# Performance work log

Measured on AMD Instinct MI355X. Metric: run time of the kernel, lower is better.

Reference implementation:

```python
import jax, jax.numpy as jnp
import numpy as np

H = 1024

def setup_inputs() -> dict:
    key = jax.random.key(0)
    ks = jax.random.split(key, 9)
    s = 1.0 / np.sqrt(H)
    x = jax.random.normal(ks[0], (4, 2048, H), dtype=jnp.float32)
    Wq = jax.random.uniform(ks[1], (H, H), jnp.float32, -s, s)
    bq = jax.random.uniform(ks[2], (H,), jnp.float32, -s, s)
    Wk = jax.random.uniform(ks[3], (H, H), jnp.float32, -s, s)
    bk = jax.random.uniform(ks[4], (H,), jnp.float32, -s, s)
    Wv = jax.random.uniform(ks[5], (H, H), jnp.float32, -s, s)
    bv = jax.random.uniform(ks[6], (H,), jnp.float32, -s, s)
    Wo = jax.random.uniform(ks[7], (H, H), jnp.float32, -s, s)
    bo = jax.random.uniform(ks[8], (H,), jnp.float32, -s, s)
    return {"x": x, "Wq": Wq, "bq": bq, "Wk": Wk, "bk": bk,
            "Wv": Wv, "bv": bv, "Wo": Wo, "bo": bo}

def reference(x, Wq, bq, Wk, bk, Wv, bv, Wo, bo):
    # Linear uses y = x @ W.T + b (torch convention: W is [out, in])
    q = jnp.einsum('bsd,ed->bse', x, Wq) + bq
    k = jnp.einsum('bsd,ed->bse', x, Wk) + bk
    v = jnp.einsum('bsd,ed->bse', x, Wv) + bv
    scale = q.shape[-1] ** 0.5
    attn = jnp.einsum('bqe,bke->bqk', q, k) / scale  # [B,S,S]
    attn = jax.nn.softmax(attn, axis=-1)
    out = jnp.einsum('bqk,bke->bqe', attn, v)
    return jnp.einsum('bse,oe->bso', out, Wo) + bo
```

## Files before the change

kernel.cpp:

```cpp
#include <hip/hip_runtime.h>

typedef short  short4v __attribute__((ext_vector_type(4)));
typedef short  short8v __attribute__((ext_vector_type(8)));
typedef __bf16 bf16x8  __attribute__((ext_vector_type(8)));
typedef float  f32x4   __attribute__((ext_vector_type(4)));
typedef float  float4v __attribute__((ext_vector_type(4)));

__device__ __forceinline__ short f2bf(float f) {
  unsigned u = __builtin_bit_cast(unsigned, f);
  u += 0x7fffu + ((u >> 16) & 1u);
  return (short)(u >> 16);
}
__device__ __forceinline__ float bf2f(short h) {
  unsigned u = ((unsigned)(unsigned short)h) << 16;
  return __builtin_bit_cast(float, u);
}
__device__ __forceinline__ bf16x8 ld8(const short* p) {
  return __builtin_bit_cast(bf16x8, *reinterpret_cast<const short8v*>(p));
}

__constant__ const float kExpScale = 0.04508422f;

__global__ __launch_bounds__(256) void k_cvt(const float* __restrict__ in,
                                             short* __restrict__ out) {
  const int i = blockIdx.x * 256 + threadIdx.x;
#pragma unroll
  for (int j = 0; j < 4; ++j) {
    const long g = (long)i + (long)j * 524288;
    float4v v = *reinterpret_cast<const float4v*>(in + g * 4);
    short4v o;
    o[0] = f2bf(v[0]); o[1] = f2bf(v[1]); o[2] = f2bf(v[2]); o[3] = f2bf(v[3]);
    *reinterpret_cast<short4v*>(out + g * 4) = o;
  }
}

__global__ __launch_bounds__(256) void k_wprep(const float* __restrict__ i0,
    const float* __restrict__ i1, const float* __restrict__ i2,
    const float* __restrict__ i3, short* __restrict__ o0, short* __restrict__ o1,
    short* __restrict__ o2, short* __restrict__ o3) {
  const int z = blockIdx.z;
  const float* in = z == 0 ? i0 : z == 1 ? i1 : z == 2 ? i2 : i3;
  short* out = z == 0 ? o0 : z == 1 ? o1 : z == 2 ? o2 : o3;
  const float sc = (z == 1) ? kExpScale : 1.0f;
  const int tid = threadIdx.x;
  const int c0 = blockIdx.x << 6;
  const int r0 = blockIdx.y << 7;
  if (z == 3) {
#pragma unroll
    for (int j = 0; j < 8; ++j) {
      int idx = j * 256 + tid;
      int r = idx >> 4, c4 = (idx & 15) << 2;
      float4v v = *reinterpret_cast<const float4v*>(in + (long)(r0 + r) * 1024 + c0 + c4);
      short4v o;
      o[0] = f2bf(v[0]); o[1] = f2bf(v[1]); o[2] = f2bf(v[2]); o[3] = f2bf(v[3]);
      *reinterpret_cast<short4v*>(out + (long)(r0 + r) * 1024 + c0 + c4) = o;
    }
    return;
  }
  __shared__ float tile[128][65];
#pragma unroll
  for (int j = 0; j < 8; ++j) {
    int idx = j * 256 + tid;
    int r = idx >> 4, c4 = (idx & 15) << 2;
    float4v v = *reinterpret_cast<const float4v*>(in + (long)(r0 + r) * 1024 + c0 + c4);
    tile[r][c4 + 0] = v[0] * sc; tile[r][c4 + 1] = v[1] * sc;
    tile[r][c4 + 2] = v[2] * sc; tile[r][c4 + 3] = v[3] * sc;
  }
  __syncthreads();
#pragma unroll
  for (int j = 0; j < 8; ++j) {
    int idx = j * 256 + tid;
    int rO = idx >> 5, g4 = (idx & 31) << 2;
    short4v o;
    o[0] = f2bf(tile[g4 + 0][rO]); o[1] = f2bf(tile[g4 + 1][rO]);
    o[2] = f2bf(tile[g4 + 2][rO]); o[3] = f2bf(tile[g4 + 3][rO]);
    *reinterpret_cast<short4v*>(out + (long)(c0 + rO) * 1024 + r0 + g4) = o;
  }
}

__device__ __forceinline__ void gemm_loop(const short* __restrict__ Ab,
    const short* __restrict__ Bb, int K, int lda, int ldb, int bm, int bn,
    f32x4 (&acc)[4][4]) {
  __shared__ __align__(16) short lsA[128 * 64];
  __shared__ __align__(16) short lsB[128 * 64];
  const int tid = threadIdx.x;
  const int lane = tid & 63, wid = tid >> 6;
  const int wr = wid >> 1, wc = wid & 1;
  const int fr = lane & 15, fq = lane >> 4;
  for (int kt = 0; kt < K; kt += 64) {
    __syncthreads();
#pragma unroll
    for (int c = 0; c < 4; ++c) {
      const int idx = c * 256 + tid;
      const int row = idx >> 3, colh = (idx & 7) << 3;
      const short* ga = Ab + (long)(bm + row) * lda + kt + colh;
      const short* gb = Bb + (long)(bn + row) * ldb + kt + colh;
      __builtin_amdgcn_global_load_lds(
          (const __attribute__((address_space(1))) void*)ga,
          (__attribute__((address_space(3))) void*)&lsA[idx * 8], 16, 0, 0);
      __builtin_amdgcn_global_load_lds(
          (const __attribute__((address_space(1))) void*)gb,
          (__attribute__((address_space(3))) void*)&lsB[idx * 8], 16, 0, 0);
    }
    __syncthreads();
#pragma unroll
    for (int ks = 0; ks < 64; ks += 32) {
      bf16x8 a[4], b[4];
#pragma unroll
      for (int m = 0; m < 4; ++m)
        a[m] = ld8(&lsA[(wr * 64 + m * 16 + fr) * 64 + ks + fq * 8]);
#pragma unroll
      for (int n = 0; n < 4; ++n)
        b[n] = ld8(&lsB[(wc * 64 + n * 16 + fr) * 64 + ks + fq * 8]);
#pragma unroll
      for (int m = 0; m < 4; ++m)
#pragma unroll
        for (int n = 0; n < 4; ++n)
          acc[m][n] = __builtin_amdgcn_mfma_f32_16x16x32_bf16(a[m], b[n], acc[m][n], 0, 0, 0);
    }
  }
}

__device__ __forceinline__ void gemm_loop_w(const short* __restrict__ Ab,
    const short* __restrict__ Bb, int K, int lda, int ldb, int bm, int bn,
    f32x4 (&acc)[4][4]) {
  __shared__ __align__(16) short lsA[128 * 64];
  __shared__ __align__(16) short lsB[256 * 64];
  const int tid = threadIdx.x;
  const int lane = tid & 63, wid = tid >> 6;
  const int wr = wid >> 2, wc = wid & 3;
  const int fr = lane & 15, fq = lane >> 4;
  for (int kt = 0; kt < K; kt += 64) {
    __syncthreads();
#pragma unroll
    for (int c = 0; c < 2; ++c) {
      const int idx = c * 512 + tid;
      const int row = idx >> 3, colh = (idx & 7) << 3;
      __builtin_amdgcn_global_load_lds(
          (const __attribute__((address_space(1))) void*)
              (Ab + (long)(bm + row) * lda + kt + colh),
          (__attribute__((address_space(3))) void*)&lsA[idx * 8], 16, 0, 0);
    }
#pragma unroll
    for (int c = 0; c < 4; ++c) {
      const int idx = c * 512 + tid;
      const int row = idx >> 3, colh = (idx & 7) << 3;
      __builtin_amdgcn_global_load_lds(
          (const __attribute__((address_space(1))) void*)
              (Bb + (long)(bn + row) * ldb + kt + colh),
          (__attribute__((address_space(3))) void*)&lsB[idx * 8], 16, 0, 0);
    }
    __syncthreads();
#pragma unroll
    for (int ks = 0; ks < 64; ks += 32) {
      bf16x8 a[4], b[4];
#pragma unroll
      for (int m = 0; m < 4; ++m)
        a[m] = ld8(&lsA[(wr * 64 + m * 16 + fr) * 64 + ks + fq * 8]);
#pragma unroll
      for (int n = 0; n < 4; ++n)
        b[n] = ld8(&lsB[(wc * 64 + n * 16 + fr) * 64 + ks + fq * 8]);
#pragma unroll
      for (int m = 0; m < 4; ++m)
#pragma unroll
        for (int n = 0; n < 4; ++n)
          acc[m][n] = __builtin_amdgcn_mfma_f32_16x16x32_bf16(a[m], b[n], acc[m][n], 0, 0, 0);
    }
  }
}

__global__ __launch_bounds__(256, 3) void k_prep2(
    const short* __restrict__ wkT, const short* __restrict__ wqT,
    const short* __restrict__ wob, const short* __restrict__ wvT,
    const float* __restrict__ bq, const float* __restrict__ Wo,
    const float* __restrict__ bv,
    short* __restrict__ mt, short* __restrict__ wv2,
    float* __restrict__ bvec, float* __restrict__ bvp) {
  const int tid = threadIdx.x;
  const int lane = tid & 63, wid = tid >> 6;
  if (blockIdx.z == 2) {
    const int r0 = (blockIdx.y * 8 + blockIdx.x) * 16;
#pragma unroll
    for (int rr = 0; rr < 4; ++rr) {
      const int row = r0 + wid * 4 + rr;
      {
        const short* xr = wkT + (long)row * 1024 + lane * 16;
        short8v a0 = *reinterpret_cast<const short8v*>(xr);
        short8v a1 = *reinterpret_cast<const short8v*>(xr + 8);
        float s = 0.f;
#pragma unroll
        for (int j = 0; j < 8; ++j) s += bf2f(a0[j]) * bq[lane * 16 + j];
#pragma unroll
        for (int j = 0; j < 8; ++j) s += bf2f(a1[j]) * bq[lane * 16 + 8 + j];
#pragma unroll
        for (int off = 32; off; off >>= 1) s += __shfl_xor(s, off);
        if (lane == 0) bvec[row] = s * kExpScale;
      }
      {
        float s = 0.f;
#pragma unroll
        for (int j = 0; j < 16; ++j)
          s += Wo[(long)row * 1024 + j * 64 + lane] * bv[j * 64 + lane];
#pragma unroll
        for (int off = 32; off; off >>= 1) s += __shfl_xor(s, off);
        if (lane == 0) bvp[row] = s;
      }
    }
    return;
  }
  const short* A = blockIdx.z == 0 ? wkT : wob;
  const short* B = blockIdx.z == 0 ? wqT : wvT;
  short* C = blockIdx.z == 0 ? mt : wv2;
  const int bm = blockIdx.x * 128, bn = blockIdx.y * 128;
  f32x4 acc[4][4] = {};
  gemm_loop(A, B, 1024, 1024, 1024, bm, bn, acc);
  const int wr = wid >> 1, wc = wid & 1;
  const int fr = lane & 15, fq = lane >> 4;
#pragma unroll
  for (int n = 0; n < 4; ++n) {
    const int col = bn + wc * 64 + n * 16 + fr;
#pragma unroll
    for (int m = 0; m < 4; ++m) {
      const int row0 = bm + wr * 64 + m * 16 + fq * 4;
#pragma unroll
      for (int i = 0; i < 4; ++i)
        C[(long)(row0 + i) * 1024 + col] = f2bf(acc[m][n][i]);
    }
  }
}

__global__ __launch_bounds__(512, 2) void k_gemmTV(
    const short* __restrict__ xb, const short* __restrict__ mt,
    const short* __restrict__ wv2, const float* __restrict__ bvp,
    const float* __restrict__ bvec, short* __restrict__ T,
    short* __restrict__ vTp, float* __restrict__ w8) {
  const int tid = threadIdx.x;
  const int lane = tid & 63, wid = tid >> 6;
  const int flat = blockIdx.x * 4 + blockIdx.y;
  if (blockIdx.z == 2) {
    const int rbase = flat * 32;
#pragma unroll
    for (int rr = 0; rr < 4; ++rr) {
      const int row = rbase + wid * 4 + rr;
      const short* xr = xb + (long)row * 1024 + lane * 16;
      short8v a0 = *reinterpret_cast<const short8v*>(xr);
      short8v a1 = *reinterpret_cast<const short8v*>(xr + 8);
      float s = 0.f;
#pragma unroll
      for (int j = 0; j < 8; ++j) s += bf2f(a0[j]) * bvec[lane * 16 + j];
#pragma unroll
      for (int j = 0; j < 8; ++j) s += bf2f(a1[j]) * bvec[lane * 16 + 8 + j];
#pragma unroll
      for (int off = 32; off; off >>= 1) s += __shfl_xor(s, off);
      if (lane == 0) w8[row] = s;
    }
    return;
  }
  const short *A, *B; const float* bias; short* C; int ldC, bm, bn;
  if (blockIdx.z == 0) {
    A = xb; B = mt; bias = nullptr; C = T; ldC = 1024;
    bm = blockIdx.x * 128; bn = blockIdx.y * 256;
  } else {
    A = wv2; B = xb; bias = bvp; C = vTp; ldC = 8192;
    bm = (flat >> 5) * 128; bn = (flat & 31) * 256;
  }
  f32x4 acc[4][4] = {};
  gemm_loop_w(A, B, 1024, 1024, 1024, bm, bn, acc);
  const int wr = wid >> 2, wc = wid & 3;
  const int fr = lane & 15, fq = lane >> 4;
#pragma unroll
  for (int n = 0; n < 4; ++n) {
    const int col = bn + wc * 64 + n * 16 + fr;
#pragma unroll
    for (int m = 0; m < 4; ++m) {
      const int row0 = bm + wr * 64 + m * 16 + fq * 4;
#pragma unroll
      for (int i = 0; i < 4; ++i) {
        const float bvr = bias ? bias[row0 + i] : 0.f;
        C[(long)(row0 + i) * ldC + col] = f2bf(acc[m][n][i] + bvr);
      }
    }
  }
}

__global__ __launch_bounds__(512, 2) void k_scores(
    const short* __restrict__ A, const short* __restrict__ B,
    const float* __restrict__ b0p, float* __restrict__ b1p,
    short* __restrict__ C0,
    int K, long sA, long sB, long sC, int ldC) {
  const int tid = threadIdx.x;
  const int lane = tid & 63, wid = tid >> 6;
  const int wr = wid >> 2, wc = wid & 3;
  const int fr = lane & 15, fq = lane >> 4;
  const int bm = blockIdx.x * 128, bn = blockIdx.y * 256;
  const int bz = blockIdx.z;

  f32x4 acc[4][4] = {};
  gemm_loop_w(A + (long)bz * sA, B + (long)bz * sB, K, K, K, bm, bn, acc);

  short* O = C0 + (long)bz * sC;
  float wv[4];
#pragma unroll
  for (int n = 0; n < 4; ++n)
    wv[n] = b0p[(long)bz * 2048 + bn + wc * 64 + n * 16 + fr];
#pragma unroll
  for (int m = 0; m < 4; ++m) {
#pragma unroll
    for (int i = 0; i < 4; ++i) {
      const int row = bm + wr * 64 + m * 16 + fq * 4 + i;
      float rs = 0.f;
#pragma unroll
      for (int n = 0; n < 4; ++n) {
        float e = exp2f(acc[m][n][i] + wv[n]);
        O[(long)row * ldC + bn + wc * 64 + n * 16 + fr] = f2bf(e);
        rs += e;
      }
      rs += __shfl_xor(rs, 1); rs += __shfl_xor(rs, 2);
      rs += __shfl_xor(rs, 4); rs += __shfl_xor(rs, 8);
      if (fr == 0)
        b1p[((long)bz * 2048 + row) * 32 + blockIdx.y * 4 + wc] = rs;
    }
  }
}

__global__ __launch_bounds__(256, 3) void k_pv(
    const short* __restrict__ A, const short* __restrict__ B,
    const float* __restrict__ b0p, float* __restrict__ b1p,
    float* __restrict__ C0,
    int K, int lda, int ldb, long sA, long sB, long sC, int ldC) {
  __shared__ float invL[128];
  const int tid = threadIdx.x;
  const int lane = tid & 63, wid = tid >> 6;
  const int wr = wid >> 1, wc = wid & 1;
  const int fr = lane & 15, fq = lane >> 4;
  const int bm = blockIdx.x * 128, bn = blockIdx.y * 128;
  const int bz = blockIdx.z;

  {
    const int row = tid >> 1, half = tid & 1;
    const float* pr = b1p + ((long)bz * 2048 + bm + row) * 32 + half * 16;
    float s = 0.f;
#pragma unroll
    for (int j = 0; j < 4; ++j) {
      float4v v = *reinterpret_cast<const float4v*>(pr + j * 4);
      s += v[0] + v[1] + v[2] + v[3];
    }
    s += __shfl_xor(s, 1);
    if (half == 0) invL[row] = 1.0f / s;
  }

  f32x4 acc[4][4] = {};
  gemm_loop(A + (long)bz * sA, B + (long)bz * sB, K, lda, ldb, bm, bn, acc);

#pragma unroll
  for (int n = 0; n < 4; ++n) {
    const int coll = wc * 64 + n * 16 + fr;
#pragma unroll
    for (int m = 0; m < 4; ++m) {
      const int rl0 = wr * 64 + m * 16 + fq * 4;
#pragma unroll
      for (int i = 0; i < 4; ++i) {
        const long row = bm + rl0 + i, col = bn + coll;
        float* O = C0 + (long)bz * sC;
        O[row * ldC + col] = acc[m][n][i] * invL[rl0 + i] + b0p[col];
      }
    }
  }
}

extern "C" void kernel_launch(void* const* d_in, const int* in_sizes, int n_in,
                              void* d_out, int out_size, void* d_ws, size_t ws_size,
                              hipStream_t stream) {
  const float* x  = (const float*)d_in[0];
  const float* Wq = (const float*)d_in[1];
  const float* bq = (const float*)d_in[2];
  const float* Wk = (const float*)d_in[3];
  const float* Wv = (const float*)d_in[5];
  const float* bv = (const float*)d_in[6];
  const float* Wo = (const float*)d_in[7];
  const float* bo = (const float*)d_in[8];

  char* ws = (char*)d_ws;
  short* xb   = (short*)ws; ws += 8192L * 1024 * 2;
  short* wkT  = (short*)ws; ws += 1024L * 1024 * 2;
  short* wob  = (short*)ws; ws += 1024L * 1024 * 2;
  short* wqT  = (short*)ws; ws += 1024L * 1024 * 2;
  short* wvT  = (short*)ws; ws += 1024L * 1024 * 2;
  short* mt   = (short*)ws; ws += 1024L * 1024 * 2;
  short* wv2  = (short*)ws; ws += 1024L * 1024 * 2;
  short* T    = (short*)ws; ws += 8192L * 1024 * 2;
  short* vTp  = (short*)ws; ws += 1024L * 8192 * 2;
  short* Sc   = (short*)ws; ws += 4L * 2048 * 2048 * 2;
  float* psum = (float*)ws; ws += 4L * 2048 * 32 * 4;
  float* w8   = (float*)ws; ws += 8192L * 4;
  float* bvec = (float*)ws; ws += 1024L * 4;
  float* bvp  = (float*)ws; ws += 1024L * 4;

  dim3 b256(256), b512(512);
  k_cvt<<<2048, b256, 0, stream>>>(x, xb);
  k_wprep<<<dim3(16, 8, 4), b256, 0, stream>>>(
      Wk, Wq, Wv, Wo, wkT, wqT, wvT, wob);
  k_prep2<<<dim3(8, 8, 3), b256, 0, stream>>>(
      wkT, wqT, wob, wvT, bq, Wo, bv, mt, wv2, bvec, bvp);
  k_gemmTV<<<dim3(64, 4, 3), b512, 0, stream>>>(
      xb, mt, wv2, bvp, bvec, T, vTp, w8);
  k_scores<<<dim3(16, 8, 4), b512, 0, stream>>>(
      T, xb, w8, psum, Sc,
      1024, 2048L * 1024, 2048L * 1024, 2048L * 2048, 2048);
  k_pv<<<dim3(16, 8, 4), b256, 0, stream>>>(
      Sc, vTp, bo, psum, (float*)d_out,
      2048, 2048, 8192, 2048L * 2048, 2048, 2048L * 1024, 1024);
}
```

Baseline: 190.8 us.

## Merge input conversion kernels and switch TV GEMM to 128x128 tiles

Fuses the x-to-bf16 conversion and weight-prep kernels into one launch by partitioning a flat grid, removing one kernel launch and its inter-kernel gap. The T/V projection GEMM moves from 512-thread 128x256 tiles to 256-thread 128x128 tiles with occupancy hint 3, doubling block count for better load balance across CUs. Smaller tiles reduce per-block reuse of operands and raise total global traffic.

New measurement: 187.3 us, median of 2. About the same (-1.8%).

```diff
diff --git a/kernel.cpp b/kernel.cpp
--- a/kernel.cpp
+++ b/kernel.cpp
@@ -21,30 +21,34 @@
 
 __constant__ const float kExpScale = 0.04508422f;
 
-__global__ __launch_bounds__(256) void k_cvt(const float* __restrict__ in,
-                                             short* __restrict__ out) {
-  const int i = blockIdx.x * 256 + threadIdx.x;
-#pragma unroll
-  for (int j = 0; j < 4; ++j) {
-    const long g = (long)i + (long)j * 524288;
-    float4v v = *reinterpret_cast<const float4v*>(in + g * 4);
-    short4v o;
-    o[0] = f2bf(v[0]); o[1] = f2bf(v[1]); o[2] = f2bf(v[2]); o[3] = f2bf(v[3]);
-    *reinterpret_cast<short4v*>(out + g * 4) = o;
-  }
-}
-
-__global__ __launch_bounds__(256) void k_wprep(const float* __restrict__ i0,
-    const float* __restrict__ i1, const float* __restrict__ i2,
-    const float* __restrict__ i3, short* __restrict__ o0, short* __restrict__ o1,
+__global__ __launch_bounds__(256) void k_inprep(
+    const float* __restrict__ x, short* __restrict__ xb,
+    const float* __restrict__ i0, const float* __restrict__ i1,
+    const float* __restrict__ i2, const float* __restrict__ i3,
+    short* __restrict__ o0, short* __restrict__ o1,
     short* __restrict__ o2, short* __restrict__ o3) {
-  const int z = blockIdx.z;
+  const int bid = blockIdx.x;
+  const int tid = threadIdx.x;
+  if (bid < 2048) {
+    const int i = bid * 256 + tid;
+#pragma unroll
+    for (int j = 0; j < 4; ++j) {
+      const long g = (long)i + (long)j * 524288;
+      float4v v = *reinterpret_cast<const float4v*>(x + g * 4);
+      short4v o;
+      o[0] = f2bf(v[0]); o[1] = f2bf(v[1]); o[2] = f2bf(v[2]); o[3] = f2bf(v[3]);
+      *reinterpret_cast<short4v*>(xb + g * 4) = o;
+    }
+    return;
+  }
+  const int w = bid - 2048;
+  const int z = w >> 7;
+  const int rem = w & 127;
+  const int c0 = (rem & 15) << 6;
+  const int r0 = (rem >> 4) << 7;
   const float* in = z == 0 ? i0 : z == 1 ? i1 : z == 2 ? i2 : i3;
   short* out = z == 0 ? o0 : z == 1 ? o1 : z == 2 ? o2 : o3;
   const float sc = (z == 1) ? kExpScale : 1.0f;
-  const int tid = threadIdx.x;
-  const int c0 = blockIdx.x << 6;
-  const int r0 = blockIdx.y << 7;
   if (z == 3) {
 #pragma unroll
     for (int j = 0; j < 8; ++j) {
@@ -229,16 +233,15 @@
   }
 }
 
-__global__ __launch_bounds__(512, 2) void k_gemmTV(
+__global__ __launch_bounds__(256, 3) void k_gemmTV(
     const short* __restrict__ xb, const short* __restrict__ mt,
     const short* __restrict__ wv2, const float* __restrict__ bvp,
     const float* __restrict__ bvec, short* __restrict__ T,
     short* __restrict__ vTp, float* __restrict__ w8) {
   const int tid = threadIdx.x;
   const int lane = tid & 63, wid = tid >> 6;
-  const int flat = blockIdx.x * 4 + blockIdx.y;
   if (blockIdx.z == 2) {
-    const int rbase = flat * 32;
+    const int rbase = (blockIdx.x * 8 + blockIdx.y) * 16;
 #pragma unroll
     for (int rr = 0; rr < 4; ++rr) {
       const int row = rbase + wid * 4 + rr;
@@ -259,14 +262,14 @@
   const short *A, *B; const float* bias; short* C; int ldC, bm, bn;
   if (blockIdx.z == 0) {
     A = xb; B = mt; bias = nullptr; C = T; ldC = 1024;
-    bm = blockIdx.x * 128; bn = blockIdx.y * 256;
+    bm = blockIdx.x * 128; bn = blockIdx.y * 128;
   } else {
     A = wv2; B = xb; bias = bvp; C = vTp; ldC = 8192;
-    bm = (flat >> 5) * 128; bn = (flat & 31) * 256;
+    bm = blockIdx.y * 128; bn = blockIdx.x * 128;
   }
   f32x4 acc[4][4] = {};
-  gemm_loop_w(A, B, 1024, 1024, 1024, bm, bn, acc);
-  const int wr = wid >> 2, wc = wid & 3;
+  gemm_loop(A, B, 1024, 1024, 1024, bm, bn, acc);
+  const int wr = wid >> 1, wc = wid & 1;
   const int fr = lane & 15, fq = lane >> 4;
 #pragma unroll
   for (int n = 0; n < 4; ++n) {
@@ -397,12 +400,11 @@
   float* bvp  = (float*)ws; ws += 1024L * 4;
 
   dim3 b256(256), b512(512);
-  k_cvt<<<2048, b256, 0, stream>>>(x, xb);
-  k_wprep<<<dim3(16, 8, 4), b256, 0, stream>>>(
-      Wk, Wq, Wv, Wo, wkT, wqT, wvT, wob);
+  k_inprep<<<2560, b256, 0, stream>>>(
+      x, xb, Wk, Wq, Wv, Wo, wkT, wqT, wvT, wob);
   k_prep2<<<dim3(8, 8, 3), b256, 0, stream>>>(
       wkT, wqT, wob, wvT, bq, Wo, bv, mt, wv2, bvec, bvp);
-  k_gemmTV<<<dim3(64, 4, 3), b512, 0, stream>>>(
+  k_gemmTV<<<dim3(64, 8, 3), b256, 0, stream>>>(
       xb, mt, wv2, bvp, bvec, T, vTp, w8);
   k_scores<<<dim3(16, 8, 4), b512, 0, stream>>>(
       T, xb, w8, psum, Sc,
```
